# Kernel optimization log

Measured on AMD Instinct MI355X. Metric: run time of the kernel, lower is better.

The kernel has to match this reference:

```python
import jax, jax.numpy as jnp
import numpy as np

KW = 31       # avg_pool kernel
PAD = 15      # padding (count_include_pad=True => divide by KW*KW always)


def _box_avg(x):
    # F.avg_pool2d(x, 31, stride=1, padding=15) with count_include_pad=True
    s = jax.lax.reduce_window(
        x, 0.0, jax.lax.add,
        window_dimensions=(1, 1, KW, KW),
        window_strides=(1, 1, 1, 1),
        padding=((0, 0), (0, 0), (PAD, PAD), (PAD, PAD)))
    return s / (KW * KW)


def setup_inputs() -> dict:
    key = jax.random.key(0)
    k1, k2 = jax.random.split(key)
    B, C, H, W = 64, 1, 512, 512
    pred = jax.random.normal(k1, (B, C, H, W), dtype=jnp.float32)
    mask = jax.random.uniform(k2, (B, C, H, W), dtype=jnp.float32)
    return {"pred": pred, "mask": mask}


def reference(pred, mask):
    weit = 1.0 + 5.0 * jnp.abs(_box_avg(mask) - mask)
    # stable BCE-with-logits, elementwise
    bce = jnp.maximum(pred, 0.0) - pred * mask + jnp.log1p(jnp.exp(-jnp.abs(pred)))
    # NOTE: original passes reduce='none' which PyTorch's legacy handling maps to
    # reduction='mean' -> wbce is a global scalar; the weit normalization cancels.
    wbce = bce.mean()  # scalar, broadcast over [B, C]
    p = jax.nn.sigmoid(pred)
    inter = (p * mask * weit).sum(axis=(2, 3))          # [B, C]
    union = ((p + mask) * weit).sum(axis=(2, 3))        # [B, C]
    wiou = 1.0 - (inter + 1.0) / (union - inter + 1.0)  # [B, C]
    return (wbce + wiou).mean()
```

## Files before the change

kernel.cpp:

```cpp
#include <hip/hip_runtime.h>
#include <math.h>

#define BDIM 64
#define HDIM 512
#define WDIM 512
#define KW   31
#define PAD  15
#define INV_KK (1.0f / 961.0f)
#define TH   64
#define NPIX ((size_t)BDIM * HDIM * WDIM)

#define NACC 129

__global__ void zero_acc_kernel(double* acc) {
    int i = threadIdx.x;
    if (i < NACC) acc[i] = 0.0;
}

template<int CTRL, int RMASK>
__device__ __forceinline__ float dpp_add(float p) {
    int t = __builtin_amdgcn_update_dpp(0, __builtin_bit_cast(int, p),
                                        CTRL, RMASK, 0xf, true);
    return p + __builtin_bit_cast(float, t);
}

__device__ __forceinline__ float wave_iscan(float p) {
    p = dpp_add<0x111, 0xf>(p);
    p = dpp_add<0x112, 0xf>(p);
    p = dpp_add<0x114, 0xf>(p);
    p = dpp_add<0x118, 0xf>(p);
    p = dpp_add<0x142, 0xa>(p);
    p = dpp_add<0x143, 0xc>(p);
    return p;
}

__device__ __forceinline__ float wave_iscan30(float p) {
    p = dpp_add<0x111, 0xf>(p);
    p = dpp_add<0x112, 0xf>(p);
    p = dpp_add<0x114, 0xf>(p);
    p = dpp_add<0x118, 0xf>(p);
    p = dpp_add<0x142, 0xa>(p);
    return p;
}

__device__ __forceinline__ float wave_shr1(float p) {
    int t = __builtin_amdgcn_update_dpp(0, __builtin_bit_cast(int, p),
                                        0x138 , 0xf, 0xf, true);
    return __builtin_bit_cast(float, t);
}

__global__ __launch_bounds__(512, 2)
void fused_kernel(const float* __restrict__ pred,
                  const float* __restrict__ mask,
                  double* __restrict__ acc) {
    __shared__ float ring[32][WDIM];
    __shared__ float red[3][8];

    const int b    = blockIdx.x;
    const int y0   = blockIdx.y * TH;
    const int x    = threadIdx.x;
    const int lane = x & 63;
    const int wv   = x >> 6;
    const int s    = wv * 64;

    const float* mbase = mask + (size_t)b * HDIM * WDIM;
    const float* pbase = pred + (size_t)b * HDIM * WDIM;

    const int acol = s - 15 + lane;
    const int bcol = s + 49 + lane;
    const bool a_ok = (acol >= 0) && (acol < WDIM);
    const bool b_ok = (lane < 30) && (bcol < WDIM);

    const int tstart = y0 - PAD;
    const int tend   = y0 + TH - 1 + PAD;

    float vs = 0.f;
    float bce_acc = 0.f, inter_acc = 0.f, uni_acc = 0.f;

    auto load_halo = [&](int row, float& A, float& B) {
        A = 0.f; B = 0.f;
        if (row >= 0 && row < HDIM) {
            const float* rp = mbase + (size_t)row * WDIM;
            if (a_ok) A = rp[acol];
            if (b_ok) B = rp[bcol];
        }
    };
    auto load_emit = [&](int row, float& M, float& P) {
        M = 0.f; P = 0.f;
        if (row >= y0 + PAD && row <= tend) {
            const size_t off = (size_t)(row - PAD) * WDIM + x;
            M = mbase[off];
            P = pbase[off];
        }
    };

    auto process = [&](int t, float A, float B, float M, float P) {
        float pa = wave_iscan(A);
        float pb = wave_iscan30(B);
        const float atot = __builtin_bit_cast(float,
            __builtin_amdgcn_readlane(__builtin_bit_cast(int, pa), 63));
        const float v1 = __shfl(pa, (lane + 30) & 63);
        const float v2 = __shfl(pb, (lane + 30) & 63);
        const float Phi = (lane <= 33) ? v1 : (atot + v2);
        const float Plo = wave_shr1(pa);
        const float hs  = Phi - Plo;

        vs += hs;
        if (t - KW >= tstart) vs -= ring[(t - KW) & 31][x];
        ring[t & 31][x] = hs;

        if (t >= y0 + PAD) {
            const float box  = vs * INV_KK;
            const float weit = 1.f + 5.f * fabsf(box - M);
            const float e1   = __expf(-fabsf(P));
            const float bce  = fmaxf(P, 0.f) - P * M + __logf(1.f + e1);
            const float sp   = __builtin_amdgcn_rcpf(1.f + __expf(-P));
            bce_acc   += bce;
            inter_acc += sp * M * weit;
            uni_acc   += (sp + M) * weit;
        }
    };

    float ca[2], cb[2], cm[2], cp[2];
    load_halo(tstart,     ca[0], cb[0]);
    load_halo(tstart + 1, ca[1], cb[1]);
    load_emit(tstart,     cm[0], cp[0]);
    load_emit(tstart + 1, cm[1], cp[1]);

    for (int t = tstart; t <= tend; t += 2) {
        float na[2], nb[2], nm[2], nq[2];
        load_halo(t + 2, na[0], nb[0]);
        load_halo(t + 3, na[1], nb[1]);
        load_emit(t + 2, nm[0], nq[0]);
        load_emit(t + 3, nm[1], nq[1]);

        process(t,     ca[0], cb[0], cm[0], cp[0]);
        process(t + 1, ca[1], cb[1], cm[1], cp[1]);

        ca[0] = na[0]; ca[1] = na[1]; cb[0] = nb[0]; cb[1] = nb[1];
        cm[0] = nm[0]; cm[1] = nm[1]; cp[0] = nq[0]; cp[1] = nq[1];
    }

#pragma unroll
    for (int off = 32; off > 0; off >>= 1) {
        bce_acc   += __shfl_down(bce_acc, off);
        inter_acc += __shfl_down(inter_acc, off);
        uni_acc   += __shfl_down(uni_acc, off);
    }
    if (lane == 0) {
        red[0][wv] = bce_acc;
        red[1][wv] = inter_acc;
        red[2][wv] = uni_acc;
    }
    __syncthreads();
    if (threadIdx.x == 0) {
        float bs = 0.f, is = 0.f, us = 0.f;
#pragma unroll
        for (int w = 0; w < 8; ++w) { bs += red[0][w]; is += red[1][w]; us += red[2][w]; }
        atomicAdd(&acc[0],      (double)bs);
        atomicAdd(&acc[1 + b],  (double)is);
        atomicAdd(&acc[65 + b], (double)us);
    }
}

__global__ void finalize_kernel(const double* __restrict__ acc, float* __restrict__ out) {
    const int b = threadIdx.x;
    double inter = acc[1 + b];
    double uni   = acc[65 + b];
    double wiou  = 1.0 - (inter + 1.0) / (uni - inter + 1.0);
#pragma unroll
    for (int off = 32; off > 0; off >>= 1) wiou += __shfl_down(wiou, off);
    if (b == 0) {
        double wbce = acc[0] / (double)NPIX;
        out[0] = (float)(wbce + wiou / (double)BDIM);
    }
}

extern "C" void kernel_launch(void* const* d_in, const int* in_sizes, int n_in,
                              void* d_out, int out_size, void* d_ws, size_t ws_size,
                              hipStream_t stream) {
    const float* pred = (const float*)d_in[0];
    const float* mask = (const float*)d_in[1];
    float* out = (float*)d_out;
    double* acc = (double*)d_ws;

    zero_acc_kernel<<<1, 256, 0, stream>>>(acc);

    dim3 grid(BDIM, HDIM / TH);
    fused_kernel<<<grid, WDIM, 0, stream>>>(pred, mask, acc);

    finalize_kernel<<<1, 64, 0, stream>>>(acc, out);
}
```

Baseline: 173.8 us.

## Swap box filter order: vertical running sum first, then horizontal wave scan

Restructures the separable box filter so each thread keeps vertical running column sums in registers, adding the incoming row and subtracting the row leaving the window by reloading it from global memory. The horizontal prefix scan then runs on those column sums, which removes the 32x512 LDS ring buffer. The halo warm-up rows are accumulated with no scan, and the scan now runs only on emitted rows. Row tile height drops to 32 and launch bounds rise to 6 blocks per CU to increase occupancy. Sigmoid now reuses the exp from the BCE term. The costs are extra global (mostly cached) reloads of the subtracted rows and more halo overhead per block from the shorter tiles.

Measured after the change: 169.1 us. -2.7%, faster.

```diff
diff --git a/kernel.cpp b/kernel.cpp
--- a/kernel.cpp
+++ b/kernel.cpp
@@ -7,7 +7,7 @@
 #define KW   31
 #define PAD  15
 #define INV_KK (1.0f / 961.0f)
-#define TH   64
+#define TH   32
 #define NPIX ((size_t)BDIM * HDIM * WDIM)
 
 #define NACC 129
@@ -49,11 +49,10 @@
     return __builtin_bit_cast(float, t);
 }
 
-__global__ __launch_bounds__(512, 2)
+__global__ __launch_bounds__(512, 6)
 void fused_kernel(const float* __restrict__ pred,
                   const float* __restrict__ mask,
                   double* __restrict__ acc) {
-    __shared__ float ring[32][WDIM];
     __shared__ float red[3][8];
 
     const int b    = blockIdx.x;
@@ -73,8 +72,9 @@
 
     const int tstart = y0 - PAD;
     const int tend   = y0 + TH - 1 + PAD;
-
-    float vs = 0.f;
+    const int smax   = (tstart > 0) ? tstart : 0;
+
+    float vsA = 0.f, vsB = 0.f;
     float bce_acc = 0.f, inter_acc = 0.f, uni_acc = 0.f;
 
     auto load_halo = [&](int row, float& A, float& B) {
@@ -85,18 +85,28 @@
             if (b_ok) B = rp[bcol];
         }
     };
+    auto load_sub = [&](int row, float& A, float& B) {
+        A = 0.f; B = 0.f;
+        if (row >= smax) {
+            const float* rp = mbase + (size_t)row * WDIM;
+            if (a_ok) A = rp[acol];
+            if (b_ok) B = rp[bcol];
+        }
+    };
     auto load_emit = [&](int row, float& M, float& P) {
         M = 0.f; P = 0.f;
-        if (row >= y0 + PAD && row <= tend) {
+        if (row <= tend) {
             const size_t off = (size_t)(row - PAD) * WDIM + x;
             M = mbase[off];
             P = pbase[off];
         }
     };
 
-    auto process = [&](int t, float A, float B, float M, float P) {
-        float pa = wave_iscan(A);
-        float pb = wave_iscan30(B);
+    auto process = [&](float A, float B, float S, float T, float M, float P) {
+        vsA += A - S;
+        vsB += B - T;
+        float pa = wave_iscan(vsA);
+        float pb = wave_iscan30(vsB);
         const float atot = __builtin_bit_cast(float,
             __builtin_amdgcn_readlane(__builtin_bit_cast(int, pa), 63));
         const float v1 = __shfl(pa, (lane + 30) & 63);
@@ -105,40 +115,50 @@
         const float Plo = wave_shr1(pa);
         const float hs  = Phi - Plo;
 
-        vs += hs;
-        if (t - KW >= tstart) vs -= ring[(t - KW) & 31][x];
-        ring[t & 31][x] = hs;
-
-        if (t >= y0 + PAD) {
-            const float box  = vs * INV_KK;
-            const float weit = 1.f + 5.f * fabsf(box - M);
-            const float e1   = __expf(-fabsf(P));
-            const float bce  = fmaxf(P, 0.f) - P * M + __logf(1.f + e1);
-            const float sp   = __builtin_amdgcn_rcpf(1.f + __expf(-P));
-            bce_acc   += bce;
-            inter_acc += sp * M * weit;
-            uni_acc   += (sp + M) * weit;
-        }
-    };
-
-    float ca[2], cb[2], cm[2], cp[2];
-    load_halo(tstart,     ca[0], cb[0]);
-    load_halo(tstart + 1, ca[1], cb[1]);
-    load_emit(tstart,     cm[0], cp[0]);
-    load_emit(tstart + 1, cm[1], cp[1]);
-
-    for (int t = tstart; t <= tend; t += 2) {
-        float na[2], nb[2], nm[2], nq[2];
-        load_halo(t + 2, na[0], nb[0]);
-        load_halo(t + 3, na[1], nb[1]);
-        load_emit(t + 2, nm[0], nq[0]);
-        load_emit(t + 3, nm[1], nq[1]);
-
-        process(t,     ca[0], cb[0], cm[0], cp[0]);
-        process(t + 1, ca[1], cb[1], cm[1], cp[1]);
-
-        ca[0] = na[0]; ca[1] = na[1]; cb[0] = nb[0]; cb[1] = nb[1];
-        cm[0] = nm[0]; cm[1] = nm[1]; cp[0] = nq[0]; cp[1] = nq[1];
+        const float box  = hs * INV_KK;
+        const float weit = 1.f + 5.f * fabsf(box - M);
+        const float e1   = __expf(-fabsf(P));
+        const float bce  = fmaxf(P, 0.f) - P * M + __logf(1.f + e1);
+        const float rr   = __builtin_amdgcn_rcpf(1.f + e1);
+        const float sp   = (P >= 0.f) ? rr : e1 * rr;
+        bce_acc   += bce;
+        inter_acc += sp * M * weit;
+        uni_acc   += (sp + M) * weit;
+    };
+
+    float cA[2], cB[2];
+    load_halo(tstart,     cA[0], cB[0]);
+    load_halo(tstart + 1, cA[1], cB[1]);
+    for (int t = tstart; t < y0 + PAD; t += 2) {
+        float nA[2], nB[2];
+        load_halo(t + 2, nA[0], nB[0]);
+        load_halo(t + 3, nA[1], nB[1]);
+        vsA += cA[0] + cA[1];
+        vsB += cB[0] + cB[1];
+        cA[0] = nA[0]; cA[1] = nA[1]; cB[0] = nB[0]; cB[1] = nB[1];
+    }
+
+    float cS[2], cT[2], cM[2], cP[2];
+    load_sub(y0 - 16, cS[0], cT[0]);
+    load_sub(y0 - 15, cS[1], cT[1]);
+    load_emit(y0 + PAD,     cM[0], cP[0]);
+    load_emit(y0 + PAD + 1, cM[1], cP[1]);
+
+    for (int t = y0 + PAD; t <= tend; t += 2) {
+        float nA[2], nB[2], nS[2], nT[2], nM[2], nP[2];
+        load_halo(t + 2, nA[0], nB[0]);
+        load_halo(t + 3, nA[1], nB[1]);
+        load_sub (t - 29, nS[0], nT[0]);
+        load_sub (t - 28, nS[1], nT[1]);
+        load_emit(t + 2, nM[0], nP[0]);
+        load_emit(t + 3, nM[1], nP[1]);
+
+        process(cA[0], cB[0], cS[0], cT[0], cM[0], cP[0]);
+        process(cA[1], cB[1], cS[1], cT[1], cM[1], cP[1]);
+
+        cA[0] = nA[0]; cA[1] = nA[1]; cB[0] = nB[0]; cB[1] = nB[1];
+        cS[0] = nS[0]; cS[1] = nS[1]; cT[0] = nT[0]; cT[1] = nT[1];
+        cM[0] = nM[0]; cM[1] = nM[1]; cP[0] = nP[0]; cP[1] = nP[1];
     }
 
 #pragma unroll
```

## Restructure box filter into per-wave strip tasks with vertical-first running sums

Applied to the files above, without the earlier changes.

Reorganizes the fused kernel so that each wave owns an 8-row by 256-column strip and each lane handles four columns with float4 loads. Vertical column sums are kept in registers as a running window, replacing the LDS ring buffer. The horizontal 31-wide sum is then taken from a wave prefix scan plus bpermute lookups. The goal is to remove LDS ring traffic, vectorize global loads and raise occupancy with smaller blocks. The cost is more halo re-reading, since each 8-row task loads 30 extra rows and subtracts rows that are re-fetched from global memory. The sigmoid is also rewritten to reuse exp(-|P|).

Result: slower. 198.6 us (+14.3%).

```diff
diff --git a/kernel.cpp b/kernel.cpp
--- a/kernel.cpp
+++ b/kernel.cpp
@@ -7,7 +7,8 @@
 #define KW   31
 #define PAD  15
 #define INV_KK (1.0f / 961.0f)
-#define TH   64
+#define TH   8
+#define SW   256
 #define NPIX ((size_t)BDIM * HDIM * WDIM)
 
 #define NACC 129
@@ -34,111 +35,156 @@
     return p;
 }
 
-__device__ __forceinline__ float wave_iscan30(float p) {
+__device__ __forceinline__ float wave_iscan8(float p) {
     p = dpp_add<0x111, 0xf>(p);
     p = dpp_add<0x112, 0xf>(p);
     p = dpp_add<0x114, 0xf>(p);
-    p = dpp_add<0x118, 0xf>(p);
-    p = dpp_add<0x142, 0xa>(p);
     return p;
 }
 
-__device__ __forceinline__ float wave_shr1(float p) {
-    int t = __builtin_amdgcn_update_dpp(0, __builtin_bit_cast(int, p),
-                                        0x138 , 0xf, 0xf, true);
-    return __builtin_bit_cast(float, t);
-}
-
-__global__ __launch_bounds__(512, 2)
+__device__ __forceinline__ float bperm(int idx, float v) {
+    return __builtin_bit_cast(float,
+        __builtin_amdgcn_ds_bpermute(idx, __builtin_bit_cast(int, v)));
+}
+
+__global__ __launch_bounds__(256, 6)
 void fused_kernel(const float* __restrict__ pred,
                   const float* __restrict__ mask,
                   double* __restrict__ acc) {
-    __shared__ float ring[32][WDIM];
-    __shared__ float red[3][8];
+    __shared__ float red[3][4];
 
     const int b    = blockIdx.x;
-    const int y0   = blockIdx.y * TH;
-    const int x    = threadIdx.x;
-    const int lane = x & 63;
-    const int wv   = x >> 6;
-    const int s    = wv * 64;
+    const int lane = threadIdx.x & 63;
+    const int wv   = threadIdx.x >> 6;
+    const int task = blockIdx.y * 4 + wv;
+    const int sx   = task & 1;
+    const int y0   = (task >> 1) * TH;
+    const int W0   = sx * SW;
 
     const float* mbase = mask + (size_t)b * HDIM * WDIM;
     const float* pbase = pred + (size_t)b * HDIM * WDIM;
 
-    const int acol = s - 15 + lane;
-    const int bcol = s + 49 + lane;
-    const bool a_ok = (acol >= 0) && (acol < WDIM);
-    const bool b_ok = (lane < 30) && (bcol < WDIM);
-
-    const int tstart = y0 - PAD;
-    const int tend   = y0 + TH - 1 + PAD;
-
-    float vs = 0.f;
+    const int acol = W0 - 16 + 4 * lane;
+    const int bcol = W0 + SW - 16 + 4 * lane;
+    const int oc   = W0 + 4 * lane;
+    const bool a_ok = (acol >= 0);
+    const bool b_ok = (lane < 8) && (bcol < WDIM);
+
+    const int iA7 = ((lane + 7)  & 63) << 2;
+    const int iA8 = ((lane + 8)  & 63) << 2;
+    const int iB0 = ((lane - 57) & 63) << 2;
+    const int iB1 = ((lane - 56) & 63) << 2;
+    const bool useB0 = (lane >= 57);
+    const bool useB1 = (lane >= 56);
+
+    const int tw0  = y0 - PAD;
+    const int smax = (tw0 > 0) ? tw0 : 0;
+
+    float4 vsA = make_float4(0.f, 0.f, 0.f, 0.f);
+    float4 vsB = make_float4(0.f, 0.f, 0.f, 0.f);
     float bce_acc = 0.f, inter_acc = 0.f, uni_acc = 0.f;
 
-    auto load_halo = [&](int row, float& A, float& B) {
-        A = 0.f; B = 0.f;
+    auto ld_AB = [&](int row, float4& A, float4& B) {
+        A = make_float4(0.f, 0.f, 0.f, 0.f);
+        B = make_float4(0.f, 0.f, 0.f, 0.f);
         if (row >= 0 && row < HDIM) {
             const float* rp = mbase + (size_t)row * WDIM;
-            if (a_ok) A = rp[acol];
-            if (b_ok) B = rp[bcol];
+            if (a_ok) A = *reinterpret_cast<const float4*>(rp + acol);
+            if (b_ok) B = *reinterpret_cast<const float4*>(rp + bcol);
         }
     };
-    auto load_emit = [&](int row, float& M, float& P) {
-        M = 0.f; P = 0.f;
-        if (row >= y0 + PAD && row <= tend) {
-            const size_t off = (size_t)(row - PAD) * WDIM + x;
-            M = mbase[off];
-            P = pbase[off];
+    auto ld_S = [&](int row, float4& S, float4& T) {
+        S = make_float4(0.f, 0.f, 0.f, 0.f);
+        T = make_float4(0.f, 0.f, 0.f, 0.f);
+        if (row >= smax) {
+            const float* rp = mbase + (size_t)row * WDIM;
+            if (a_ok) S = *reinterpret_cast<const float4*>(rp + acol);
+            if (b_ok) T = *reinterpret_cast<const float4*>(rp + bcol);
         }
     };
-
-    auto process = [&](int t, float A, float B, float M, float P) {
-        float pa = wave_iscan(A);
-        float pb = wave_iscan30(B);
-        const float atot = __builtin_bit_cast(float,
-            __builtin_amdgcn_readlane(__builtin_bit_cast(int, pa), 63));
-        const float v1 = __shfl(pa, (lane + 30) & 63);
-        const float v2 = __shfl(pb, (lane + 30) & 63);
-        const float Phi = (lane <= 33) ? v1 : (atot + v2);
-        const float Plo = wave_shr1(pa);
-        const float hs  = Phi - Plo;
-
-        vs += hs;
-        if (t - KW >= tstart) vs -= ring[(t - KW) & 31][x];
-        ring[t & 31][x] = hs;
-
-        if (t >= y0 + PAD) {
-            const float box  = vs * INV_KK;
-            const float weit = 1.f + 5.f * fabsf(box - M);
-            const float e1   = __expf(-fabsf(P));
-            const float bce  = fmaxf(P, 0.f) - P * M + __logf(1.f + e1);
-            const float sp   = __builtin_amdgcn_rcpf(1.f + __expf(-P));
-            bce_acc   += bce;
-            inter_acc += sp * M * weit;
-            uni_acc   += (sp + M) * weit;
-        }
-    };
-
-    float ca[2], cb[2], cm[2], cp[2];
-    load_halo(tstart,     ca[0], cb[0]);
-    load_halo(tstart + 1, ca[1], cb[1]);
-    load_emit(tstart,     cm[0], cp[0]);
-    load_emit(tstart + 1, cm[1], cp[1]);
-
-    for (int t = tstart; t <= tend; t += 2) {
-        float na[2], nb[2], nm[2], nq[2];
-        load_halo(t + 2, na[0], nb[0]);
-        load_halo(t + 3, na[1], nb[1]);
-        load_emit(t + 2, nm[0], nq[0]);
-        load_emit(t + 3, nm[1], nq[1]);
-
-        process(t,     ca[0], cb[0], cm[0], cp[0]);
-        process(t + 1, ca[1], cb[1], cm[1], cp[1]);
-
-        ca[0] = na[0]; ca[1] = na[1]; cb[0] = nb[0]; cb[1] = nb[1];
-        cm[0] = nm[0]; cm[1] = nm[1]; cp[0] = nq[0]; cp[1] = nq[1];
+    auto ld_P = [&](int yo, float4& Pv) {
+        Pv = make_float4(0.f, 0.f, 0.f, 0.f);
+        if (yo < HDIM)
+            Pv = *reinterpret_cast<const float4*>(pbase + (size_t)yo * WDIM + oc);
+    };
+    auto ld_M = [&](int yo, float4& Mv) {
+        Mv = *reinterpret_cast<const float4*>(mbase + (size_t)yo * WDIM + oc);
+    };
+
+    auto emit1 = [&](float hs, float M, float P) {
+        const float box  = hs * INV_KK;
+        const float weit = 1.f + 5.f * fabsf(box - M);
+        const float e1   = __expf(-fabsf(P));
+        const float bce  = fmaxf(P, 0.f) - P * M + __logf(1.f + e1);
+        const float rr   = __builtin_amdgcn_rcpf(1.f + e1);
+        const float sp   = (P >= 0.f) ? rr : e1 * rr;
+        bce_acc   += bce;
+        inter_acc += sp * M * weit;
+        uni_acc   += (sp + M) * weit;
+    };
+
+    float4 cA, cB, nP;
+    ld_AB(tw0, cA, cB);
+    ld_P(y0, nP);
+
+#pragma unroll 1
+    for (int i = 0; i < 30; ++i) {
+        float4 nA, nB;
+        ld_AB(tw0 + i + 1, nA, nB);
+        vsA.x += cA.x; vsA.y += cA.y; vsA.z += cA.z; vsA.w += cA.w;
+        vsB.x += cB.x; vsB.y += cB.y; vsB.z += cB.z; vsB.w += cB.w;
+        cA = nA; cB = nB;
+    }
+
+#pragma unroll 1
+    for (int i = 0; i < TH; ++i) {
+        const int t  = y0 + PAD + i;
+        const int yo = y0 + i;
+
+        const float4 cP = nP;
+        ld_P(yo + 1, nP);
+        float4 sA4, sB4, M4;
+        ld_S(t - KW, sA4, sB4);
+        ld_M(yo, M4);
+        const float4 tA = cA, tB = cB;
+        ld_AB(t + 1, cA, cB);
+
+        vsA.x += tA.x - sA4.x; vsA.y += tA.y - sA4.y;
+        vsA.z += tA.z - sA4.z; vsA.w += tA.w - sA4.w;
+        vsB.x += tB.x - sB4.x; vsB.y += tB.y - sB4.y;
+        vsB.z += tB.z - sB4.z; vsB.w += tB.w - sB4.w;
+
+        const float pA0 = vsA.x, pA1 = pA0 + vsA.y,
+                    pA2 = pA1 + vsA.z, pA3 = pA2 + vsA.w;
+        const float pB0 = vsB.x, pB1 = pB0 + vsB.y,
+                    pB2 = pB1 + vsB.z, pB3 = pB2 + vsB.w;
+
+        const float SA  = wave_iscan(pA3);
+        const float Aex = SA - pA3;
+        const float PA0 = Aex + pA0, PA1 = Aex + pA1,
+                    PA2 = Aex + pA2, PA3 = SA;
+        const float Atot = __builtin_bit_cast(float,
+            __builtin_amdgcn_readlane(__builtin_bit_cast(int, SA), 63));
+
+        const float SB  = wave_iscan8(pB3);
+        const float Bex = Atot + (SB - pB3);
+        const float PB0 = Bex + pB0, PB1 = Bex + pB1,
+                    PB2 = Bex + pB2, PB3 = Bex + pB3;
+
+        const float hA0 = bperm(iA7, PA3), hB0 = bperm(iB0, PB3);
+        const float hA1 = bperm(iA8, PA0), hB1 = bperm(iB1, PB0);
+        const float hA2 = bperm(iA8, PA1), hB2 = bperm(iB1, PB1);
+        const float hA3 = bperm(iA8, PA2), hB3 = bperm(iB1, PB2);
+
+        const float hs0 = (useB0 ? hB0 : hA0) - PA0;
+        const float hs1 = (useB1 ? hB1 : hA1) - PA1;
+        const float hs2 = (useB1 ? hB2 : hA2) - PA2;
+        const float hs3 = (useB1 ? hB3 : hA3) - PA3;
+
+        emit1(hs0, M4.x, cP.x);
+        emit1(hs1, M4.y, cP.y);
+        emit1(hs2, M4.z, cP.z);
+        emit1(hs3, M4.w, cP.w);
     }
 
 #pragma unroll
@@ -156,7 +202,7 @@
     if (threadIdx.x == 0) {
         float bs = 0.f, is = 0.f, us = 0.f;
 #pragma unroll
-        for (int w = 0; w < 8; ++w) { bs += red[0][w]; is += red[1][w]; us += red[2][w]; }
+        for (int w = 0; w < 4; ++w) { bs += red[0][w]; is += red[1][w]; us += red[2][w]; }
         atomicAdd(&acc[0],      (double)bs);
         atomicAdd(&acc[1 + b],  (double)is);
         atomicAdd(&acc[65 + b], (double)us);
@@ -186,8 +232,8 @@
 
     zero_acc_kernel<<<1, 256, 0, stream>>>(acc);
 
-    dim3 grid(BDIM, HDIM / TH);
-    fused_kernel<<<grid, WDIM, 0, stream>>>(pred, mask, acc);
+    dim3 grid(BDIM, (HDIM / TH) * 2 / 4);
+    fused_kernel<<<grid, 256, 0, stream>>>(pred, mask, acc);
 
     finalize_kernel<<<1, 64, 0, stream>>>(acc, out);
 }
```
